# Performance work log

Hardware: AMD Instinct MI355X
Metric: run time of the kernel (lower is better)

## Reference

```python
import jax, jax.numpy as jnp
import numpy as np

N, E, G = 100000, 400000, 2000
D = 128            # dim_node
DE = 128 + 300     # dim_edge after RBF concat
NC = 300           # RBF centers
CUT_LO, CUT_HI = 0.0, 30.0
N_CONV = 3


def setup_inputs() -> dict:
    key = jax.random.key(0)
    ks = jax.random.split(key, 32)
    inp = {}
    inp['Z'] = jax.random.randint(ks[0], (N,), 0, 20)
    inp['edge_type'] = jax.random.randint(ks[1], (E,), 0, 400)
    inp['dist'] = jax.random.uniform(ks[2], (E,), dtype=jnp.float32) * CUT_HI
    inp['src'] = jax.random.randint(ks[3], (E,), 0, N)
    inp['dst'] = jax.random.randint(ks[4], (E,), 0, N)
    inp['graph_ids'] = jnp.sort(jax.random.randint(ks[5], (N,), 0, G))
    s = 0.05
    inp['node_emb'] = jax.random.normal(ks[6], (20, D), jnp.float32) * s
    inp['edge_emb'] = jax.random.normal(ks[7], (400, D), jnp.float32) * s
    # per-conv-layer weights, stacked over layer dim
    inp['Wn1'] = jax.random.normal(ks[8], (N_CONV, D, D), jnp.float32) * s
    inp['bn1'] = jnp.zeros((N_CONV, D), jnp.float32)
    inp['Wn2'] = jax.random.normal(ks[9], (N_CONV, D, D), jnp.float32) * s
    inp['bn2'] = jnp.zeros((N_CONV, D), jnp.float32)
    inp['We1'] = jax.random.normal(ks[10], (N_CONV, DE, DE), jnp.float32) * s
    inp['be1'] = jnp.zeros((N_CONV, DE), jnp.float32)
    inp['We2'] = jax.random.normal(ks[11], (N_CONV, D, DE), jnp.float32) * s
    inp['be2'] = jnp.zeros((N_CONV, D), jnp.float32)
    inp['Wc'] = jax.random.normal(ks[12], (N_CONV, D, D), jnp.float32) * s
    inp['bc'] = jnp.zeros((N_CONV, D), jnp.float32)
    # read layer
    inp['Wr1'] = jax.random.normal(ks[13], (D, D), jnp.float32) * s
    inp['br1'] = jnp.zeros((D,), jnp.float32)
    inp['Wr2'] = jax.random.normal(ks[14], (1, D), jnp.float32) * s
    inp['br2'] = jnp.zeros((1,), jnp.float32)
    return inp


def _rbf(dist):
    centers = jnp.linspace(CUT_LO, CUT_HI, NC, dtype=jnp.float32)
    gap = centers[1] - centers[0]
    # [E, NC]
    return jnp.exp(-((dist[:, None] - centers[None, :]) ** 2) / gap)


def reference(Z, edge_type, dist, src, dst, graph_ids,
              node_emb, edge_emb,
              Wn1, bn1, Wn2, bn2, We1, be1, We2, be2, Wc, bc,
              Wr1, br1, Wr2, br2):
    h = node_emb[Z]                          # [N, D] node embedding
    e = edge_emb[edge_type]                  # [E, D] edge embedding
    e = jnp.concatenate([e, _rbf(dist)], axis=1)   # [E, DE]
    for i in range(N_CONV):
        hs = h[src]                          # gather src node feats [E, D]
        hn = jax.nn.relu(hs @ Wn1[i].T + bn1[i]) @ Wn2[i].T + bn2[i]   # [E, D]
        ee = jax.nn.relu(e @ We1[i].T + be1[i]) @ We2[i].T + be2[i]    # [E, D]
        m = jnp.tanh((hn * ee) @ Wc[i].T + bc[i])                      # [E, D]
        h = h + jax.ops.segment_sum(m, dst, num_segments=N)            # scatter-sum
    r = jax.nn.relu(h @ Wr1.T + br1) @ Wr2.T + br2                     # [N, 1]
    out = jax.ops.segment_sum(r, graph_ids, num_segments=G)            # [G, 1]
    return out.flatten()                                               # [G]
```

## Files before the change

### kernel.cpp

```cpp
#include <hip/hip_runtime.h>

#define NN 100000
#define En 400000
#define Gn 2000
#define GRID 2048

typedef unsigned short u16;
typedef unsigned int u32;
typedef _Float16 f16;
typedef f16 f16x8 __attribute__((ext_vector_type(8)));
typedef f16 f16x4 __attribute__((ext_vector_type(4)));
typedef float f32x4 __attribute__((ext_vector_type(4)));

__device__ __forceinline__ void lds_barrier() {
  asm volatile("s_waitcnt lgkmcnt(0)\ns_barrier" ::: "memory");
}

#define MFMA16(a, b, c) __builtin_amdgcn_mfma_f32_16x16x32_f16(a, b, c, 0, 0, 0)


__global__ __launch_bounds__(256) void k_prepw(
    const float* __restrict__ Wn1, const float* __restrict__ Wn2,
    const float* __restrict__ Wc, const float* __restrict__ We2,
    const float* __restrict__ We1,
    f16* __restrict__ Wn1b, f16* __restrict__ Wn2b, f16* __restrict__ Wcb,
    f16* __restrict__ We2b, f16* __restrict__ Rb, u32* __restrict__ hist) {
  int i = blockIdx.x * 256 + threadIdx.x;
  if (i < 49152) {
    Wn1b[i] = (f16)Wn1[i];
  } else if (i < 98304) {
    int j = i - 49152;
    Wn2b[j] = (f16)Wn2[j];
  } else if (i < 147456) {
    int j = i - 98304;
    Wcb[j] = (f16)Wc[j];
  } else if (i < 319488) {
    int j = i - 147456;
    int l = j / 57344;
    int r = j - l * 57344;
    int row = r / 448;
    int k = r - row * 448;
    float v = (k < 428) ? We2[l * 54784 + row * 428 + k] : 0.f;
    We2b[j] = (f16)v;
  } else if (i < 749568) {
    int j = i - 319488;
    int l = j / 143360;
    int r = j - l * 143360;
    int row = r / 320;
    int k = r - row * 320;
    float v = 0.f;
    if (row < 428 && k < 300) v = We1[(size_t)l * 183184 + row * 428 + 128 + k];
    Rb[j] = (f16)v;
  } else if (i < 849568) {
    hist[i - 749568] = 0u;
  }
}


__global__ __launch_bounds__(256) void k_t2(const float* __restrict__ edge_emb,
                                            const float* __restrict__ We1,
                                            const float* __restrict__ be1,
                                            f16* __restrict__ T2) {
  __shared__ __align__(16) f16 sA[64 * 136];
  __shared__ __align__(16) f16 sB[128 * 136];
  const int tid = threadIdx.x;
  const int l = blockIdx.x / 28;
  const int rb = blockIdx.x - l * 28;
  const int tb = rb >> 2, jb = rb & 3;
  const int t0 = tb * 64, j0 = jb * 128;
  for (int i = tid; i < 64 * 32; i += 256) {
    int e = i >> 5, c = (i & 31) * 4;
    int t = t0 + e;
    float4 v = make_float4(0.f, 0.f, 0.f, 0.f);
    if (t < 400) v = *(const float4*)&edge_emb[t * 128 + c];
    f16x4 o = {(f16)v.x, (f16)v.y, (f16)v.z, (f16)v.w};
    *(f16x4*)&sA[e * 136 + c] = o;
  }
  for (int i = tid; i < 128 * 32; i += 256) {
    int rr = i >> 5, c = (i & 31) * 4;
    int j = j0 + rr;
    float4 v = make_float4(0.f, 0.f, 0.f, 0.f);
    if (j < 428) v = *(const float4*)&We1[(size_t)l * 183184 + j * 428 + c];
    f16x4 o = {(f16)v.x, (f16)v.y, (f16)v.z, (f16)v.w};
    *(f16x4*)&sB[rr * 136 + c] = o;
  }
  lds_barrier();
  const int lane = tid & 63, wave = tid >> 6;
  const int q = lane >> 4, ln = lane & 15;
  const int nb = wave * 32;

  f32x4 acc[4][2];
#pragma unroll
  for (int m = 0; m < 4; ++m)
#pragma unroll
    for (int n = 0; n < 2; ++n) acc[m][n] = 0.f;
#pragma unroll
  for (int k0 = 0; k0 < 128; k0 += 32) {
    f16x8 a[4];
#pragma unroll
    for (int m = 0; m < 4; ++m)
      a[m] = *(const f16x8*)&sA[(m * 16 + ln) * 136 + k0 + q * 8];
#pragma unroll
    for (int n = 0; n < 2; ++n) {
      f16x8 b = *(const f16x8*)&sB[(nb + n * 16 + ln) * 136 + k0 + q * 8];
#pragma unroll
      for (int m = 0; m < 4; ++m) acc[m][n] = MFMA16(a[m], b, acc[m][n]);
    }
  }
#pragma unroll
  for (int n = 0; n < 2; ++n) {
    int col = nb + n * 16 + ln;
    int gj = j0 + col;
    float bb = (gj < 428) ? be1[l * 428 + gj] : 0.f;
#pragma unroll
    for (int m = 0; m < 4; ++m)
#pragma unroll
      for (int r = 0; r < 4; ++r) {
        int row = m * 16 + q * 4 + r;
        int t = t0 + row;
        if (t < 400 && gj < 448) {
          float s = acc[m][n][r] + bb;
          T2[l * 179200 + t * 448 + gj] = (gj < 428) ? (f16)s : (f16)0.f;
        }
      }
  }
}

__global__ __launch_bounds__(256) void k_dtab(const f16* __restrict__ Rb,
                                              f16* __restrict__ Dtab) {
  const int tid = threadIdx.x;
  int l = blockIdx.x / (GRID + 1);
  int g = blockIdx.x - l * (GRID + 1);
  float d = (float)g * (30.f / (float)GRID);
  int kc = (int)(d * (299.f / 30.f) + 0.5f);
  int kk0 = min(max(kc - 20, 0), 280) & ~7;
  __shared__ float sE[40];
  if (tid < 40) {
    float x = d - (float)(kk0 + tid) * (30.f / 299.f);
    sE[tid] = __expf(-x * x * (299.f / 30.f));
  }
  __syncthreads();
  for (int j = tid; j < 448; j += 256) {
    const f16* rr = &Rb[((size_t)l * 448 + j) * 320 + kk0];
    float s = 0.f;
#pragma unroll
    for (int v = 0; v < 5; ++v) {
      f16x8 rv = *(const f16x8*)&rr[v * 8];
#pragma unroll
      for (int t = 0; t < 8; ++t) s += sE[v * 8 + t] * (float)rv[t];
    }
    Dtab[((size_t)(l * (GRID + 1) + g)) * 448 + j] = (f16)s;
  }
}


__global__ __launch_bounds__(256) void k_hist(const int* __restrict__ dstv,
                                              u32* __restrict__ hist) {
  int e = blockIdx.x * 256 + threadIdx.x;
  if (e < En) atomicAdd(&hist[dstv[e]], 1u);
}

__global__ __launch_bounds__(1024) void k_scan1(const u32* __restrict__ hist,
                                                u32* __restrict__ excl,
                                                u32* __restrict__ part) {
  __shared__ u32 ws[16];
  const int t = threadIdx.x, b = blockIdx.x, i = b * 1024 + t;
  const int lane = t & 63, wid = t >> 6;
  u32 v = (i < NN) ? hist[i] : 0u;
  u32 acc = v;
#pragma unroll
  for (int off = 1; off < 64; off <<= 1) {
    u32 x = __shfl_up(acc, off);
    if (lane >= off) acc += x;
  }
  if (lane == 63) ws[wid] = acc;
  __syncthreads();
  if (t < 16) {
    u32 wa = ws[t];
#pragma unroll
    for (int off = 1; off < 16; off <<= 1) {
      u32 x = __shfl_up(wa, off);
      if (t >= off) wa += x;
    }
    ws[t] = wa;
  }
  __syncthreads();
  u32 base = (wid > 0) ? ws[wid - 1] : 0u;
  u32 inc = base + acc;
  if (i < NN) excl[i] = inc - v;
  if (t == 1023) part[b] = inc;
}

__global__ __launch_bounds__(128) void k_scan2(u32* __restrict__ part, int n) {
  __shared__ u32 s[128];
  const int t = threadIdx.x;
  u32 v = (t < n) ? part[t] : 0u;
  s[t] = v;
  __syncthreads();
  u32 acc = v;
  for (int off = 1; off < 128; off <<= 1) {
    u32 add = (t >= off) ? s[t - off] : 0u;
    __syncthreads();
    acc += add;
    s[t] = acc;
    __syncthreads();
  }
  if (t < n) part[t] = acc - v;
}

__global__ __launch_bounds__(1024) void k_scan3(const u32* __restrict__ excl,
                                                const u32* __restrict__ part,
                                                u32* __restrict__ cursor) {
  int i = blockIdx.x * 1024 + threadIdx.x;
  if (i < NN) cursor[i] = excl[i] + part[blockIdx.x];
}

__global__ __launch_bounds__(256) void k_scatter(const int* __restrict__ etype,
                                                 const float* __restrict__ dist,
                                                 const int* __restrict__ srcv,
                                                 const int* __restrict__ dstv,
                                                 u32* __restrict__ cursor,
                                                 int4* __restrict__ epack,
                                                 int* __restrict__ edst) {
  int e = blockIdx.x * 256 + threadIdx.x;
  if (e >= En) return;
  int d = dstv[e];
  int pos = (int)atomicAdd(&cursor[d], 1u);
  float fi = dist[e] * ((float)GRID / 30.f);
  int ix = (int)(fi + 0.5f);
  epack[pos] = make_int4(srcv[e], etype[e] * 448, ix * 448, 0);
  edst[pos] = d;
}


__global__ __launch_bounds__(256) void k_node(const float* __restrict__ h,
                                              const f16* __restrict__ W1,
                                              const float* __restrict__ b1,
                                              const f16* __restrict__ W2,
                                              const float* __restrict__ b2,
                                              f16* __restrict__ n2) {
  __shared__ __align__(16) f16 sH[64 * 136];
  __shared__ __align__(16) f16 sT[64 * 136];
  const int tid = threadIdx.x;
  const int nbase = blockIdx.x * 64;
  for (int i = tid; i < 64 * 32; i += 256) {
    int e = i >> 5, c = (i & 31) * 4;
    int node = nbase + e;
    float4 v = make_float4(0.f, 0.f, 0.f, 0.f);
    if (node < NN) v = *(const float4*)&h[(size_t)node * 128 + c];
    f16x4 o = {(f16)v.x, (f16)v.y, (f16)v.z, (f16)v.w};
    *(f16x4*)&sH[e * 136 + c] = o;
  }
  lds_barrier();
  const int lane = tid & 63, wave = tid >> 6;
  const int q = lane >> 4, ln = lane & 15;
  const int nb = wave * 32;

  f32x4 acc[4][2];
#pragma unroll
  for (int m = 0; m < 4; ++m)
#pragma unroll
    for (int n = 0; n < 2; ++n) acc[m][n] = 0.f;
#pragma unroll
  for (int k0 = 0; k0 < 128; k0 += 32) {
    f16x8 a[4];
#pragma unroll
    for (int m = 0; m < 4; ++m)
      a[m] = *(const f16x8*)&sH[(m * 16 + ln) * 136 + k0 + q * 8];
#pragma unroll
    for (int n = 0; n < 2; ++n) {
      f16x8 b = *(const f16x8*)&W1[(nb + n * 16 + ln) * 128 + k0 + q * 8];
#pragma unroll
      for (int m = 0; m < 4; ++m) acc[m][n] = MFMA16(a[m], b, acc[m][n]);
    }
  }
#pragma unroll
  for (int n = 0; n < 2; ++n) {
    int col = nb + n * 16 + ln;
    float bb = b1[col];
#pragma unroll
    for (int m = 0; m < 4; ++m)
#pragma unroll
      for (int r = 0; r < 4; ++r) {
        int row = m * 16 + q * 4 + r;
        sT[row * 136 + col] = (f16)fmaxf(acc[m][n][r] + bb, 0.f);
      }
  }
  lds_barrier();

  f32x4 acc2[4][2];
#pragma unroll
  for (int m = 0; m < 4; ++m)
#pragma unroll
    for (int n = 0; n < 2; ++n) acc2[m][n] = 0.f;
#pragma unroll
  for (int k0 = 0; k0 < 128; k0 += 32) {
    f16x8 a[4];
#pragma unroll
    for (int m = 0; m < 4; ++m)
      a[m] = *(const f16x8*)&sT[(m * 16 + ln) * 136 + k0 + q * 8];
#pragma unroll
    for (int n = 0; n < 2; ++n) {
      f16x8 b = *(const f16x8*)&W2[(nb + n * 16 + ln) * 128 + k0 + q * 8];
#pragma unroll
      for (int m = 0; m < 4; ++m) acc2[m][n] = MFMA16(a[m], b, acc2[m][n]);
    }
  }
#pragma unroll
  for (int n = 0; n < 2; ++n) {
    int col = nb + n * 16 + ln;
    float bb = b2[col];
#pragma unroll
    for (int m = 0; m < 4; ++m)
#pragma unroll
      for (int r = 0; r < 4; ++r) {
        int row = m * 16 + q * 4 + r;
        int node = nbase + row;
        if (node < NN) n2[(size_t)node * 128 + col] = (f16)(acc2[m][n][r] + bb);
      }
  }
}


__global__ __launch_bounds__(256) void k_node0(const int* __restrict__ Z,
                                               const float* __restrict__ node_emb,
                                               const f16* __restrict__ W1,
                                               const float* __restrict__ b1,
                                               const f16* __restrict__ W2,
                                               const float* __restrict__ b2,
                                               f16* __restrict__ n2,
                                               float* __restrict__ h,
                                               float* __restrict__ out) {
  __shared__ __align__(16) f16 sH[64 * 136];
  __shared__ __align__(16) f16 sT[64 * 136];
  __shared__ int sZ[64];
  const int tid = threadIdx.x;
  const int nbase = blockIdx.x * 64;
  {
    int oi = blockIdx.x * 256 + tid;
    if (oi < Gn) out[oi] = 0.f;
  }
  if (tid < 64) sZ[tid] = Z[min(nbase + tid, NN - 1)];
  lds_barrier();
  for (int i = tid; i < 64 * 32; i += 256) {
    int e = i >> 5, c = (i & 31) * 4;
    int node = nbase + e;
    float4 v = *(const float4*)&node_emb[sZ[e] * 128 + c];
    f16x4 o = {(f16)v.x, (f16)v.y, (f16)v.z, (f16)v.w};
    *(f16x4*)&sH[e * 136 + c] = o;
    if (node < NN) *(float4*)&h[(size_t)node * 128 + c] = v;
  }
  lds_barrier();
  const int lane = tid & 63, wave = tid >> 6;
  const int q = lane >> 4, ln = lane & 15;
  const int nb = wave * 32;

  f32x4 acc[4][2];
#pragma unroll
  for (int m = 0; m < 4; ++m)
#pragma unroll
    for (int n = 0; n < 2; ++n) acc[m][n] = 0.f;
#pragma unroll
  for (int k0 = 0; k0 < 128; k0 += 32) {
    f16x8 a[4];
#pragma unroll
    for (int m = 0; m < 4; ++m)
      a[m] = *(const f16x8*)&sH[(m * 16 + ln) * 136 + k0 + q * 8];
#pragma unroll
    for (int n = 0; n < 2; ++n) {
      f16x8 b = *(const f16x8*)&W1[(nb + n * 16 + ln) * 128 + k0 + q * 8];
#pragma unroll
      for (int m = 0; m < 4; ++m) acc[m][n] = MFMA16(a[m], b, acc[m][n]);
    }
  }
#pragma unroll
  for (int n = 0; n < 2; ++n) {
    int col = nb + n * 16 + ln;
    float bb = b1[col];
#pragma unroll
    for (int m = 0; m < 4; ++m)
#pragma unroll
      for (int r = 0; r < 4; ++r) {
        int row = m * 16 + q * 4 + r;
        sT[row * 136 + col] = (f16)fmaxf(acc[m][n][r] + bb, 0.f);
      }
  }
  lds_barrier();

  f32x4 acc2[4][2];
#pragma unroll
  for (int m = 0; m < 4; ++m)
#pragma unroll
    for (int n = 0; n < 2; ++n) acc2[m][n] = 0.f;
#pragma unroll
  for (int k0 = 0; k0 < 128; k0 += 32) {
    f16x8 a[4];
#pragma unroll
    for (int m = 0; m < 4; ++m)
      a[m] = *(const f16x8*)&sT[(m * 16 + ln) * 136 + k0 + q * 8];
#pragma unroll
    for (int n = 0; n < 2; ++n) {
      f16x8 b = *(const f16x8*)&W2[(nb + n * 16 + ln) * 128 + k0 + q * 8];
#pragma unroll
      for (int m = 0; m < 4; ++m) acc2[m][n] = MFMA16(a[m], b, acc2[m][n]);
    }
  }
#pragma unroll
  for (int n = 0; n < 2; ++n) {
    int col = nb + n * 16 + ln;
    float bb = b2[col];
#pragma unroll
    for (int m = 0; m < 4; ++m)
#pragma unroll
      for (int r = 0; r < 4; ++r) {
        int row = m * 16 + q * 4 + r;
        int node = nbase + row;
        if (node < NN) n2[(size_t)node * 128 + col] = (f16)(acc2[m][n][r] + bb);
      }
  }
}


__global__ __launch_bounds__(256)
__attribute__((amdgpu_waves_per_eu(4, 4))) void k_edge(
    const int4* __restrict__ epack, const int* __restrict__ edst,
    const f16* __restrict__ T2, const f16* __restrict__ Dtab,
    const f16* __restrict__ We2b, const float* __restrict__ be2,
    const f16* __restrict__ Wcb, const float* __restrict__ bc,
    const f16* __restrict__ n2, float* __restrict__ h) {
  __shared__ __align__(16) f16 sC[2][64 * 136];
  __shared__ int sSrc[64], sDst[64], sT2o[64], sIdx[64];

  const int tid = threadIdx.x;
  const int e0 = blockIdx.x * 64;
  if (tid < 64) {
    int4 p = epack[e0 + tid];
    sSrc[tid] = p.x;
    sT2o[tid] = p.y;
    sIdx[tid] = p.z;
    sDst[tid] = edst[e0 + tid];
  }
  lds_barrier();

  const int lane = tid & 63, wave = tid >> 6;
  const int q = lane >> 4, ln = lane & 15;
  const int nb = wave * 32;

  f32x4 acc[4][2];
#pragma unroll
  for (int m = 0; m < 4; ++m)
#pragma unroll
    for (int n = 0; n < 2; ++n) acc[m][n] = 0.f;

  auto add_relu = [](f16x8 lo, f16x8 t2) -> f16x8 {
    f16x8 v = t2 + lo;
    f16x8 z = {};
    return __builtin_elementwise_max(v, z);
  };
  auto pfD128 = [&](int k0, f16x8* plo) {
    const int cg = tid & 15, eb = tid >> 4;
    const int col = k0 + cg * 8;
#pragma unroll
    for (int i = 0; i < 4; ++i)
      plo[i] = *(const f16x8*)&Dtab[sIdx[eb + i * 16] + col];
  };
  auto pfT128 = [&](int k0, f16x8* pt2) {
    const int cg = tid & 15, eb = tid >> 4;
    const int col = k0 + cg * 8;
#pragma unroll
    for (int i = 0; i < 4; ++i)
      pt2[i] = *(const f16x8*)&T2[sT2o[eb + i * 16] + col];
  };
  auto st128 = [&](f16* buf, const f16x8* plo, const f16x8* pt2) {
    const int cg = tid & 15, eb = tid >> 4;
#pragma unroll
    for (int i = 0; i < 4; ++i) {
      int e = eb + i * 16;
      *(f16x8*)&buf[e * 136 + cg * 8] = add_relu(plo[i], pt2[i]);
    }
  };
  auto pfD64 = [&](f16x8* plo) {
    const int cg = tid & 7, eb = tid >> 3;
    const int col = 384 + cg * 8;
#pragma unroll
    for (int i = 0; i < 2; ++i)
      plo[i] = *(const f16x8*)&Dtab[sIdx[eb + i * 32] + col];
  };
  auto pfT64 = [&](f16x8* pt2) {
    const int cg = tid & 7, eb = tid >> 3;
    const int col = 384 + cg * 8;
#pragma unroll
    for (int i = 0; i < 2; ++i)
      pt2[i] = *(const f16x8*)&T2[sT2o[eb + i * 32] + col];
  };
  auto st64 = [&](f16* buf, const f16x8* plo, const f16x8* pt2) {
    const int cg = tid & 7, eb = tid >> 3;
#pragma unroll
    for (int i = 0; i < 2; ++i) {
      int e = eb + i * 32;
      *(f16x8*)&buf[e * 136 + cg * 8] = add_relu(plo[i], pt2[i]);
    }
  };
  auto mfma_chunk = [&](const f16* buf, int k0, int nk) {
    for (int kk = 0; kk < nk; ++kk) {
      f16x8 a[4];
#pragma unroll
      for (int m = 0; m < 4; ++m)
        a[m] = *(const f16x8*)&buf[(m * 16 + ln) * 136 + kk * 32 + q * 8];
#pragma unroll
      for (int n = 0; n < 2; ++n) {
        f16x8 b = *(const f16x8*)&We2b[(nb + n * 16 + ln) * 448 + k0 + kk * 32 + q * 8];
#pragma unroll
        for (int m = 0; m < 4; ++m) acc[m][n] = MFMA16(a[m], b, acc[m][n]);
      }
    }
  };

  f16x8 dA[4], dB[4], tc[4];
  f16x8 d64[2], t64[2];

  pfD128(0, dA);
  pfT128(0, tc);
  pfD128(128, dB);
  st128(sC[0], dA, tc);
  lds_barrier();

  pfT128(128, tc);
  pfD128(256, dA);
  mfma_chunk(sC[0], 0, 4);
  st128(sC[1], dB, tc);
  lds_barrier();

  pfT128(256, tc);
  pfD64(d64);
  mfma_chunk(sC[1], 128, 4);
  st128(sC[0], dA, tc);
  lds_barrier();

  f16x8 nrows[4];
  pfT64(t64);
#pragma unroll
  for (int i = 0; i < 4; ++i) {
    int u = tid + 256 * i;
    int e = u >> 4, cg = u & 15;
    nrows[i] = *(const f16x8*)&n2[(size_t)sSrc[e] * 128 + cg * 8];
  }
  mfma_chunk(sC[0], 256, 4);
  st64(sC[1], d64, t64);
  lds_barrier();

  f16* sN = sC[0];
#pragma unroll
  for (int i = 0; i < 4; ++i) {
    int u = tid + 256 * i;
    int e = u >> 4, cg = u & 15;
    *(f16x8*)&sN[e * 136 + cg * 8] = nrows[i];
  }
  mfma_chunk(sC[1], 384, 2);
  lds_barrier();

  f16* sP = sC[1];
  {
    float be2v[2] = {be2[nb + ln], be2[nb + 16 + ln]};
#pragma unroll
    for (int n = 0; n < 2; ++n) {
      int col = nb + n * 16 + ln;
#pragma unroll
      for (int m = 0; m < 4; ++m)
#pragma unroll
        for (int r = 0; r < 4; ++r) {
          int row = m * 16 + q * 4 + r;
          float ee = acc[m][n][r] + be2v[n];
          sP[row * 136 + col] = (f16)(ee * (float)sN[row * 136 + col]);
        }
    }
  }
  lds_barrier();

  {
    f32x4 acc2[4][2];
#pragma unroll
    for (int m = 0; m < 4; ++m)
#pragma unroll
      for (int n = 0; n < 2; ++n) acc2[m][n] = 0.f;
#pragma unroll
    for (int k0 = 0; k0 < 128; k0 += 32) {
      f16x8 a[4];
#pragma unroll
      for (int m = 0; m < 4; ++m)
        a[m] = *(const f16x8*)&sP[(m * 16 + ln) * 136 + k0 + q * 8];
#pragma unroll
      for (int n = 0; n < 2; ++n) {
        f16x8 b = *(const f16x8*)&Wcb[(nb + n * 16 + ln) * 128 + k0 + q * 8];
#pragma unroll
        for (int m = 0; m < 4; ++m) acc2[m][n] = MFMA16(a[m], b, acc2[m][n]);
      }
    }
    float bcv[2] = {bc[nb + ln], bc[nb + 16 + ln]};
#pragma unroll
    for (int m = 0; m < 4; ++m) {
      int d[4];
#pragma unroll
      for (int r = 0; r < 4; ++r) d[r] = sDst[m * 16 + q * 4 + r];
#pragma unroll
      for (int n = 0; n < 2; ++n) {
        int col = nb + n * 16 + ln;
        float tv[4];
#pragma unroll
        for (int r = 0; r < 4; ++r) {
          float x = acc2[m][n][r] + bcv[n];
          x = fminf(2.f, fmaxf(-2.f, x));
          float x2 = x * x;
          tv[r] = x * (15.f + x2) * __builtin_amdgcn_rcpf(15.f + 6.f * x2);
        }
        float s = tv[0];
        int cur = d[0];
#pragma unroll
        for (int r = 1; r < 4; ++r) {
          if (d[r] == cur) {
            s += tv[r];
          } else {
            unsafeAtomicAdd(&h[(size_t)cur * 128 + col], s);
            cur = d[r];
            s = tv[r];
          }
        }
        unsafeAtomicAdd(&h[(size_t)cur * 128 + col], s);
      }
    }
  }
}


__global__ __launch_bounds__(256) void k_read(const float* __restrict__ h,
                                              const float* __restrict__ Wr1,
                                              const float* __restrict__ br1,
                                              const float* __restrict__ Wr2,
                                              const float* __restrict__ br2,
                                              const int* __restrict__ gid,
                                              float* __restrict__ out) {
  __shared__ __align__(16) f16 sH[64 * 136];
  __shared__ __align__(16) f16 sW[128 * 136];
  __shared__ float sR4[4][64];
  const int tid = threadIdx.x;
  const int nbase = blockIdx.x * 64;
  for (int i = tid; i < 64 * 32; i += 256) {
    int e = i >> 5, c = (i & 31) * 4;
    int node = nbase + e;
    float4 v = make_float4(0.f, 0.f, 0.f, 0.f);
    if (node < NN) v = *(const float4*)&h[(size_t)node * 128 + c];
    f16x4 o = {(f16)v.x, (f16)v.y, (f16)v.z, (f16)v.w};
    *(f16x4*)&sH[e * 136 + c] = o;
  }
  for (int i = tid; i < 128 * 32; i += 256) {
    int rr = i >> 5, c = (i & 31) * 4;
    float4 v = *(const float4*)&Wr1[rr * 128 + c];
    f16x4 o = {(f16)v.x, (f16)v.y, (f16)v.z, (f16)v.w};
    *(f16x4*)&sW[rr * 136 + c] = o;
  }
  lds_barrier();
  const int lane = tid & 63, wave = tid >> 6;
  const int q = lane >> 4, ln = lane & 15;
  const int nb = wave * 32;

  f32x4 acc[4][2];
#pragma unroll
  for (int m = 0; m < 4; ++m)
#pragma unroll
    for (int n = 0; n < 2; ++n) acc[m][n] = 0.f;
#pragma unroll
  for (int k0 = 0; k0 < 128; k0 += 32) {
    f16x8 a[4];
#pragma unroll
    for (int m = 0; m < 4; ++m)
      a[m] = *(const f16x8*)&sH[(m * 16 + ln) * 136 + k0 + q * 8];
#pragma unroll
    for (int n = 0; n < 2; ++n) {
      f16x8 b = *(const f16x8*)&sW[(nb + n * 16 + ln) * 136 + k0 + q * 8];
#pragma unroll
      for (int m = 0; m < 4; ++m) acc[m][n] = MFMA16(a[m], b, acc[m][n]);
    }
  }
#pragma unroll
  for (int m = 0; m < 4; ++m)
#pragma unroll
    for (int r = 0; r < 4; ++r) {
      float t = 0.f;
#pragma unroll
      for (int n = 0; n < 2; ++n) {
        int col = nb + n * 16 + ln;
        t += fmaxf(acc[m][n][r] + br1[col], 0.f) * Wr2[col];
      }
      t += __shfl_xor(t, 1);
      t += __shfl_xor(t, 2);
      t += __shfl_xor(t, 4);
      t += __shfl_xor(t, 8);
      if (ln == 0) sR4[wave][m * 16 + q * 4 + r] = t;
    }
  lds_barrier();
  if (tid < 64) {
    int node = nbase + tid;
    if (node < NN) {
      float s = sR4[0][tid] + sR4[1][tid] + sR4[2][tid] + sR4[3][tid] + br2[0];
      unsafeAtomicAdd(&out[gid[node]], s);
    }
  }
}


extern "C" void kernel_launch(void* const* d_in, const int* in_sizes, int n_in,
                              void* d_out, int out_size, void* d_ws, size_t ws_size,
                              hipStream_t stream) {
  const int* Z = (const int*)d_in[0];
  const int* etype = (const int*)d_in[1];
  const float* dist = (const float*)d_in[2];
  const int* src = (const int*)d_in[3];
  const int* dst = (const int*)d_in[4];
  const int* gid = (const int*)d_in[5];
  const float* node_emb = (const float*)d_in[6];
  const float* edge_emb = (const float*)d_in[7];
  const float* Wn1 = (const float*)d_in[8];
  const float* bn1 = (const float*)d_in[9];
  const float* Wn2 = (const float*)d_in[10];
  const float* bn2 = (const float*)d_in[11];
  const float* We1 = (const float*)d_in[12];
  const float* be1 = (const float*)d_in[13];
  const float* We2 = (const float*)d_in[14];
  const float* be2 = (const float*)d_in[15];
  const float* Wc = (const float*)d_in[16];
  const float* bc = (const float*)d_in[17];
  const float* Wr1 = (const float*)d_in[18];
  const float* br1 = (const float*)d_in[19];
  const float* Wr2 = (const float*)d_in[20];
  const float* br2 = (const float*)d_in[21];
  float* out = (float*)d_out;

  char* ws = (char*)d_ws;
  float* h = (float*)(ws);
  f16* n2 = (f16*)(ws + 51200000);
  f16* Rb = (f16*)(ws + 76800000);
  f16* We2b = (f16*)(ws + 77660160);
  f16* Wcb = (f16*)(ws + 78004224);
  f16* Wn1b = (f16*)(ws + 78102528);
  f16* Wn2b = (f16*)(ws + 78200832);
  f16* T2 = (f16*)(ws + 78299136);
  f16* Dtab = (f16*)(ws + 79374336);
  int4* epack = (int4*)(ws + 84882048);
  int* edst = (int*)(ws + 91282048);
  u32* hist = (u32*)(ws + 92882048);
  u32* cursor = (u32*)(ws + 93282048);
  u32* excl = (u32*)(ws + 93682048);
  u32* part = (u32*)(ws + 94082048);

  k_prepw<<<3319, 256, 0, stream>>>(Wn1, Wn2, Wc, We2, We1,
                                    Wn1b, Wn2b, Wcb, We2b, Rb, hist);
  k_hist<<<1563, 256, 0, stream>>>(dst, hist);
  k_scan1<<<98, 1024, 0, stream>>>(hist, excl, part);
  k_scan2<<<1, 128, 0, stream>>>(part, 98);
  k_scan3<<<98, 1024, 0, stream>>>(excl, part, cursor);
  k_scatter<<<1563, 256, 0, stream>>>(etype, dist, src, dst, cursor, epack, edst);

  k_t2<<<84, 256, 0, stream>>>(edge_emb, We1, be1, T2);
  k_dtab<<<3 * (GRID + 1), 256, 0, stream>>>(Rb, Dtab);

  for (int l = 0; l < 3; ++l) {
    if (l == 0) {
      k_node0<<<1563, 256, 0, stream>>>(Z, node_emb, Wn1b, bn1, Wn2b, bn2,
                                        n2, h, out);
    } else {
      k_node<<<1563, 256, 0, stream>>>(h, Wn1b + l * 16384, bn1 + l * 128,
                                       Wn2b + l * 16384, bn2 + l * 128, n2);
    }
    k_edge<<<6250, 256, 0, stream>>>(epack, edst,
                                     T2 + l * 179200, Dtab + (size_t)l * (GRID + 1) * 448,
                                     We2b + l * 57344, be2 + l * 128,
                                     Wcb + l * 16384, bc + l * 128, n2, h);
  }
  k_read<<<1563, 256, 0, stream>>>(h, Wr1, br1, Wr2, br2, gid, out);
}
```

Measured before the change: 833.4 us.

## Fold scan2 into scan3, pack dst into epack, deepen edge prefetch

```diff
diff --git a/kernel.cpp b/kernel.cpp
--- a/kernel.cpp
+++ b/kernel.cpp
@@ -191,28 +191,23 @@
   if (t == 1023) part[b] = inc;
 }
 
-__global__ __launch_bounds__(128) void k_scan2(u32* __restrict__ part, int n) {
-  __shared__ u32 s[128];
-  const int t = threadIdx.x;
-  u32 v = (t < n) ? part[t] : 0u;
-  s[t] = v;
-  __syncthreads();
-  u32 acc = v;
-  for (int off = 1; off < 128; off <<= 1) {
-    u32 add = (t >= off) ? s[t - off] : 0u;
-    __syncthreads();
-    acc += add;
-    s[t] = acc;
-    __syncthreads();
-  }
-  if (t < n) part[t] = acc - v;
-}
-
 __global__ __launch_bounds__(1024) void k_scan3(const u32* __restrict__ excl,
                                                 const u32* __restrict__ part,
                                                 u32* __restrict__ cursor) {
-  int i = blockIdx.x * 1024 + threadIdx.x;
-  if (i < NN) cursor[i] = excl[i] + part[blockIdx.x];
+  __shared__ u32 sW[2];
+  __shared__ u32 sBase;
+  const int t = threadIdx.x, b = blockIdx.x;
+  if (t < 128) {
+    u32 v = (t < b) ? part[t] : 0u;
+#pragma unroll
+    for (int off = 32; off > 0; off >>= 1) v += __shfl_down(v, off);
+    if ((t & 63) == 0) sW[t >> 6] = v;
+  }
+  __syncthreads();
+  if (t == 0) sBase = sW[0] + sW[1];
+  __syncthreads();
+  int i = b * 1024 + t;
+  if (i < NN) cursor[i] = excl[i] + sBase;
 }
 
 __global__ __launch_bounds__(256) void k_scatter(const int* __restrict__ etype,
@@ -220,16 +215,14 @@
                                                  const int* __restrict__ srcv,
                                                  const int* __restrict__ dstv,
                                                  u32* __restrict__ cursor,
-                                                 int4* __restrict__ epack,
-                                                 int* __restrict__ edst) {
+                                                 int4* __restrict__ epack) {
   int e = blockIdx.x * 256 + threadIdx.x;
   if (e >= En) return;
   int d = dstv[e];
   int pos = (int)atomicAdd(&cursor[d], 1u);
   float fi = dist[e] * ((float)GRID / 30.f);
   int ix = (int)(fi + 0.5f);
-  epack[pos] = make_int4(srcv[e], etype[e] * 448, ix * 448, 0);
-  edst[pos] = d;
+  epack[pos] = make_int4(srcv[e], etype[e] * 448, ix * 448, d);
 }
 
 
@@ -422,8 +415,8 @@
 
 
 __global__ __launch_bounds__(256)
-__attribute__((amdgpu_waves_per_eu(4, 4))) void k_edge(
-    const int4* __restrict__ epack, const int* __restrict__ edst,
+__attribute__((amdgpu_waves_per_eu(3, 3))) void k_edge(
+    const int4* __restrict__ epack,
     const f16* __restrict__ T2, const f16* __restrict__ Dtab,
     const f16* __restrict__ We2b, const float* __restrict__ be2,
     const f16* __restrict__ Wcb, const float* __restrict__ bc,
@@ -438,7 +431,7 @@
     sSrc[tid] = p.x;
     sT2o[tid] = p.y;
     sIdx[tid] = p.z;
-    sDst[tid] = edst[e0 + tid];
+    sDst[tid] = p.w;
   }
   lds_barrier();
 
@@ -516,29 +509,29 @@
     }
   };
 
-  f16x8 dA[4], dB[4], tc[4];
+  f16x8 dA[4], tA[4], dB[4], tB[4];
   f16x8 d64[2], t64[2];
 
   pfD128(0, dA);
-  pfT128(0, tc);
+  pfT128(0, tA);
   pfD128(128, dB);
-  st128(sC[0], dA, tc);
-  lds_barrier();
-
-  pfT128(128, tc);
+  pfT128(128, tB);
+  st128(sC[0], dA, tA);
+  lds_barrier();
+
   pfD128(256, dA);
+  pfT128(256, tA);
   mfma_chunk(sC[0], 0, 4);
-  st128(sC[1], dB, tc);
-  lds_barrier();
-
-  pfT128(256, tc);
+  st128(sC[1], dB, tB);
+  lds_barrier();
+
   pfD64(d64);
+  pfT64(t64);
   mfma_chunk(sC[1], 128, 4);
-  st128(sC[0], dA, tc);
+  st128(sC[0], dA, tA);
   lds_barrier();
 
   f16x8 nrows[4];
-  pfT64(t64);
 #pragma unroll
   for (int i = 0; i < 4; ++i) {
     int u = tid + 256 * i;
@@ -746,7 +739,6 @@
   f16* T2 = (f16*)(ws + 78299136);
   f16* Dtab = (f16*)(ws + 79374336);
   int4* epack = (int4*)(ws + 84882048);
-  int* edst = (int*)(ws + 91282048);
   u32* hist = (u32*)(ws + 92882048);
   u32* cursor = (u32*)(ws + 93282048);
   u32* excl = (u32*)(ws + 93682048);
@@ -756,9 +748,8 @@
                                     Wn1b, Wn2b, Wcb, We2b, Rb, hist);
   k_hist<<<1563, 256, 0, stream>>>(dst, hist);
   k_scan1<<<98, 1024, 0, stream>>>(hist, excl, part);
-  k_scan2<<<1, 128, 0, stream>>>(part, 98);
   k_scan3<<<98, 1024, 0, stream>>>(excl, part, cursor);
-  k_scatter<<<1563, 256, 0, stream>>>(etype, dist, src, dst, cursor, epack, edst);
+  k_scatter<<<1563, 256, 0, stream>>>(etype, dist, src, dst, cursor, epack);
 
   k_t2<<<84, 256, 0, stream>>>(edge_emb, We1, be1, T2);
   k_dtab<<<3 * (GRID + 1), 256, 0, stream>>>(Rb, Dtab);
@@ -771,7 +762,7 @@
       k_node<<<1563, 256, 0, stream>>>(h, Wn1b + l * 16384, bn1 + l * 128,
                                        Wn2b + l * 16384, bn2 + l * 128, n2);
     }
-    k_edge<<<6250, 256, 0, stream>>>(epack, edst,
+    k_edge<<<6250, 256, 0, stream>>>(epack,
                                      T2 + l * 179200, Dtab + (size_t)l * (GRID + 1) * 448,
                                      We2b + l * 57344, be2 + l * 128,
                                      Wcb + l * 16384, bc + l * 128, n2, h);
```

Measured after the change: 872.4 us. +4.7%, slower.
